# Kernel tuning notes

Measured on AMD Instinct MI355X. Metric: run time of the kernel, lower is better.

## Reference

```python
import jax, jax.numpy as jnp
import numpy as np

B, T, D = 32, 1024, 512
G, K = 8, 256          # num_groups, codes_per_group
GD = D // G            # group_dim = 64


def setup_inputs() -> dict:
    key = jax.random.key(0)
    k_x, k_cb = jax.random.split(key)
    x = jax.random.normal(k_x, (B, T, D), dtype=jnp.float32)
    # nn.Embedding weights init uniform_(-1/K, 1/K), one table per group -> [G, K, GD]
    codebooks = jax.random.uniform(k_cb, (G, K, GD), dtype=jnp.float32,
                                   minval=-1.0 / K, maxval=1.0 / K)
    return {"x": x, "codebooks": codebooks}


def reference(x, codebooks):
    Bx, Tx, Dx = x.shape
    xg = x.reshape(Bx, Tx, G, GD)                      # [B,T,G,gd]
    # squared euclidean distances to each code, per group: [B,T,G,K]
    x_sq = jnp.sum(xg ** 2, axis=-1, keepdims=True)    # [B,T,G,1]
    c_sq = jnp.sum(codebooks ** 2, axis=-1)            # [G,K]
    xc = jnp.einsum('btgd,gkd->btgk', xg, codebooks)   # [B,T,G,K]
    d = x_sq + c_sq[None, None] - 2.0 * xc
    idx = jnp.argmin(d, axis=-1)                       # [B,T,G] int
    # gather selected codes: codebooks[g, idx[b,t,g]] -> [B,T,G,gd]
    xq = jnp.take_along_axis(codebooks[None, None],    # [1,1,G,K,gd]
                             idx[..., None, None], axis=3).squeeze(3)
    sg = jax.lax.stop_gradient
    # per-group mse means (over B,T,gd), summed over groups (matches torch loop)
    losses = (jnp.sum(jnp.mean((sg(xq) - xg) ** 2, axis=(0, 1, 3)))
              + jnp.sum(jnp.mean((xq - sg(xg)) ** 2, axis=(0, 1, 3))))
    # straight-through estimator
    xq_st = xg + sg(xq - xg)
    x_q = xq_st.reshape(Bx, Tx, Dx)
    return x_q, losses, idx
```

## Files before the change

### kernel.cpp

```cpp
#include <hip/hip_runtime.h>

#define BT_TOTAL (32 * 1024)
#define DIM 512
#define NG 8
#define NK 256
#define GD 64

#define XQ_ELEMS (BT_TOTAL * DIM)
#define LOSS_OFF XQ_ELEMS
#define IDX_OFF (XQ_ELEMS + 1)

__global__ void pq_prep(const float* __restrict__ cb,
                        float* __restrict__ csq,
                        float* __restrict__ loss_slot) {
    int i = blockIdx.x * 256 + threadIdx.x;
    if (i == 0) *loss_slot = 0.0f;
    if (i < NG * NK) {
        const float* row = cb + (size_t)i * GD;
        float a0 = 0.f, a1 = 0.f, a2 = 0.f, a3 = 0.f;
#pragma unroll
        for (int d = 0; d < GD; d += 4) {
            a0 = fmaf(row[d + 0], row[d + 0], a0);
            a1 = fmaf(row[d + 1], row[d + 1], a1);
            a2 = fmaf(row[d + 2], row[d + 2], a2);
            a3 = fmaf(row[d + 3], row[d + 3], a3);
        }
        csq[i] = (a0 + a1) + (a2 + a3);
    }
}

__global__ __launch_bounds__(256) void pq_main(const float* __restrict__ x,
                                               const float* __restrict__ cb,
                                               const float* __restrict__ csq,
                                               float* __restrict__ out) {
    const int g = blockIdx.y;
    const int bt = blockIdx.x * 256 + threadIdx.x;

    const float* xrow = x + (size_t)bt * DIM + g * GD;
    float4 xr[16];
#pragma unroll
    for (int i = 0; i < 16; ++i) xr[i] = ((const float4*)xrow)[i];

    float a0 = 0.f, a1 = 0.f, a2 = 0.f, a3 = 0.f;
#pragma unroll
    for (int i = 0; i < 16; ++i) {
        a0 = fmaf(xr[i].x, xr[i].x, a0);
        a1 = fmaf(xr[i].y, xr[i].y, a1);
        a2 = fmaf(xr[i].z, xr[i].z, a2);
        a3 = fmaf(xr[i].w, xr[i].w, a3);
    }
    const float x_sq = (a0 + a1) + (a2 + a3);

    const float* cbg = cb + (size_t)g * NK * GD;
    const float* csqg = csq + g * NK;

    float best = 3.402823466e38f;
    int bi = 0;
    for (int k = 0; k < NK; ++k) {
        const float4* c4 = (const float4*)(cbg + k * GD);
        float d0 = 0.f, d1 = 0.f, d2 = 0.f, d3 = 0.f;
#pragma unroll
        for (int i = 0; i < 16; ++i) {
            float4 c = c4[i];
            d0 = fmaf(xr[i].x, c.x, d0);
            d1 = fmaf(xr[i].y, c.y, d1);
            d2 = fmaf(xr[i].z, c.z, d2);
            d3 = fmaf(xr[i].w, c.w, d3);
        }
        float dot = (d0 + d1) + (d2 + d3);
        float dist = (x_sq + csqg[k]) - 2.0f * dot;
        if (dist < best) { best = dist; bi = k; }
    }

    out[IDX_OFF + (size_t)bt * NG + g] = (float)bi;

    const float4* q4 = (const float4*)(cbg + bi * GD);
    float4* xq_out = (float4*)(out + (size_t)bt * DIM + g * GD);
    float s0 = 0.f, s1 = 0.f, s2 = 0.f, s3 = 0.f;
#pragma unroll
    for (int i = 0; i < 16; ++i) {
        float4 q = q4[i];
        float dx = q.x - xr[i].x;
        float dy = q.y - xr[i].y;
        float dz = q.z - xr[i].z;
        float dw = q.w - xr[i].w;
        float4 o;
        o.x = xr[i].x + dx;
        o.y = xr[i].y + dy;
        o.z = xr[i].z + dz;
        o.w = xr[i].w + dw;
        xq_out[i] = o;
        s0 = fmaf(dx, dx, s0);
        s1 = fmaf(dy, dy, s1);
        s2 = fmaf(dz, dz, s2);
        s3 = fmaf(dw, dw, s3);
    }
    float part = (s0 + s1) + (s2 + s3);

#pragma unroll
    for (int off = 32; off > 0; off >>= 1) part += __shfl_down(part, off);

    __shared__ float wsum[4];
    const int lane = threadIdx.x & 63;
    const int wid = threadIdx.x >> 6;
    if (lane == 0) wsum[wid] = part;
    __syncthreads();
    if (threadIdx.x == 0) {
        float bs = (wsum[0] + wsum[1]) + (wsum[2] + wsum[3]);
        atomicAdd(out + LOSS_OFF, bs * (2.0f / 2097152.0f));
    }
}

extern "C" void kernel_launch(void* const* d_in, const int* in_sizes, int n_in,
                              void* d_out, int out_size, void* d_ws, size_t ws_size,
                              hipStream_t stream) {
    const float* x = (const float*)d_in[0];
    const float* cb = (const float*)d_in[1];
    float* out = (float*)d_out;
    float* csq = (float*)d_ws;

    pq_prep<<<dim3(8), dim3(256), 0, stream>>>(cb, csq, out + LOSS_OFF);

    dim3 grid(BT_TOTAL / 256, NG);
    pq_main<<<grid, dim3(256), 0, stream>>>(x, cb, csq, out);
}
```

Baseline: 147.7 us.

## Split codebook search across two half-blocks and coalesce output writes

Each block now handles 128 rows, with two thread halves each scanning half of the 256 codes, merging the argmin through shared memory. This doubles the grid and the parallelism available for the latency-bound scan. The epilogue is restructured so 16 threads cooperatively write each row's 64 floats, giving coalesced stores instead of each thread writing its own row. It also sets a min-blocks launch bound and partially unrolls the code loop. The cost is reloading x from global memory in the epilogue, plus extra barriers.

```diff
diff --git a/kernel.cpp b/kernel.cpp
--- a/kernel.cpp
+++ b/kernel.cpp
@@ -5,6 +5,7 @@
 #define NG 8
 #define NK 256
 #define GD 64
+#define QB 128
 
 #define XQ_ELEMS (BT_TOTAL * DIM)
 #define LOSS_OFF XQ_ELEMS
@@ -29,12 +30,20 @@
     }
 }
 
-__global__ __launch_bounds__(256) void pq_main(const float* __restrict__ x,
-                                               const float* __restrict__ cb,
-                                               const float* __restrict__ csq,
-                                               float* __restrict__ out) {
+__global__ __launch_bounds__(256, 4) void pq_main(const float* __restrict__ x,
+                                                  const float* __restrict__ cb,
+                                                  const float* __restrict__ csq,
+                                                  float* __restrict__ out) {
     const int g = blockIdx.y;
-    const int bt = blockIdx.x * 256 + threadIdx.x;
+    const int t = threadIdx.x;
+    const int kh = __builtin_amdgcn_readfirstlane(t >> 7);
+    const int ql = t & (QB - 1);
+    const int q0 = blockIdx.x * QB;
+    const int bt = q0 + ql;
+
+    __shared__ float m_d[QB];
+    __shared__ int   m_i[QB];
+    __shared__ float wsum[4];
 
     const float* xrow = x + (size_t)bt * DIM + g * GD;
     float4 xr[16];
@@ -54,9 +63,12 @@
     const float* cbg = cb + (size_t)g * NK * GD;
     const float* csqg = csq + g * NK;
 
+    const int kbase = kh << 7;
     float best = 3.402823466e38f;
-    int bi = 0;
-    for (int k = 0; k < NK; ++k) {
+    int bi = kbase;
+#pragma unroll 2
+    for (int kk = 0; kk < 128; ++kk) {
+        const int k = kbase + kk;
         const float4* c4 = (const float4*)(cbg + k * GD);
         float d0 = 0.f, d1 = 0.f, d2 = 0.f, d3 = 0.f;
 #pragma unroll
@@ -72,24 +84,37 @@
         if (dist < best) { best = dist; bi = k; }
     }
 
-    out[IDX_OFF + (size_t)bt * NG + g] = (float)bi;
+    if (kh == 1) { m_d[ql] = best; m_i[ql] = bi; }
+    __syncthreads();
+    if (kh == 0) {
+        float dh = m_d[ql];
+        int ih = m_i[ql];
+        if (dh < best) { best = dh; bi = ih; }
+        m_i[ql] = bi;
+        out[IDX_OFF + (size_t)bt * NG + g] = (float)bi;
+    }
+    __syncthreads();
 
-    const float4* q4 = (const float4*)(cbg + bi * GD);
-    float4* xq_out = (float4*)(out + (size_t)bt * DIM + g * GD);
+    const int r_off = t >> 4;
+    const int c4i = t & 15;
     float s0 = 0.f, s1 = 0.f, s2 = 0.f, s3 = 0.f;
 #pragma unroll
-    for (int i = 0; i < 16; ++i) {
-        float4 q = q4[i];
-        float dx = q.x - xr[i].x;
-        float dy = q.y - xr[i].y;
-        float dz = q.z - xr[i].z;
-        float dw = q.w - xr[i].w;
+    for (int p = 0; p < 8; ++p) {
+        const int r = p * 16 + r_off;
+        const int code = m_i[r];
+        const size_t base = (size_t)(q0 + r) * DIM + g * GD + c4i * 4;
+        float4 x4 = *(const float4*)(x + base);
+        float4 q4 = *(const float4*)(cbg + code * GD + c4i * 4);
+        float dx = q4.x - x4.x;
+        float dy = q4.y - x4.y;
+        float dz = q4.z - x4.z;
+        float dw = q4.w - x4.w;
         float4 o;
-        o.x = xr[i].x + dx;
-        o.y = xr[i].y + dy;
-        o.z = xr[i].z + dz;
-        o.w = xr[i].w + dw;
-        xq_out[i] = o;
+        o.x = x4.x + dx;
+        o.y = x4.y + dy;
+        o.z = x4.z + dz;
+        o.w = x4.w + dw;
+        *(float4*)(out + base) = o;
         s0 = fmaf(dx, dx, s0);
         s1 = fmaf(dy, dy, s1);
         s2 = fmaf(dz, dz, s2);
@@ -100,12 +125,11 @@
 #pragma unroll
     for (int off = 32; off > 0; off >>= 1) part += __shfl_down(part, off);
 
-    __shared__ float wsum[4];
-    const int lane = threadIdx.x & 63;
-    const int wid = threadIdx.x >> 6;
+    const int lane = t & 63;
+    const int wid = t >> 6;
     if (lane == 0) wsum[wid] = part;
     __syncthreads();
-    if (threadIdx.x == 0) {
+    if (t == 0) {
         float bs = (wsum[0] + wsum[1]) + (wsum[2] + wsum[3]);
         atomicAdd(out + LOSS_OFF, bs * (2.0f / 2097152.0f));
     }
@@ -121,6 +145,6 @@
 
     pq_prep<<<dim3(8), dim3(256), 0, stream>>>(cb, csq, out + LOSS_OFF);
 
-    dim3 grid(BT_TOTAL / 256, NG);
+    dim3 grid(BT_TOTAL / QB, NG);
     pq_main<<<grid, dim3(256), 0, stream>>>(x, cb, csq, out);
 }
```

Result: no change. 147.5 us (-0.1%).
